# Kernel tuning notes

Hardware: AMD Instinct MI355X
Metric: run time of the kernel (lower is better)

Reference implementation:

```python
import jax, jax.numpy as jnp
import numpy as np

B, D, N = 16, 512, 1024


def setup_inputs() -> dict:
    key = jax.random.key(0)
    k1, k2, k3, k4, k5 = jax.random.split(key, 5)
    return {
        "src_embedding": jax.random.normal(k1, (B, D, N), dtype=jnp.float32),
        "tgt_embedding": jax.random.normal(k2, (B, D, N), dtype=jnp.float32),
        "src": jax.random.normal(k3, (B, 3, N), dtype=jnp.float32),
        "tgt": jax.random.normal(k4, (B, 3, N), dtype=jnp.float32),
        "temperature": jax.random.uniform(k5, (B,), dtype=jnp.float32),
    }


def reference(src_embedding, tgt_embedding, src, tgt, temperature):
    b, d, n = src_embedding.shape
    # scores = softmax(temp * (src_emb^T tgt_emb) / sqrt(d_k), dim=2)
    logits = jnp.einsum("bdn,bdm->bnm", src_embedding, tgt_embedding) / np.sqrt(d).astype(np.float32)
    scores = jax.nn.softmax(temperature.reshape(b, 1, 1) * logits, axis=2)  # [B,N,N]
    # src_corr = tgt @ scores^T  -> soft correspondences [B,3,N]
    src_corr = jnp.einsum("bdm,bnm->bdn", tgt, scores)
    src_mean = src.mean(axis=2, keepdims=True)            # [B,3,1]
    corr_mean = src_corr.mean(axis=2, keepdims=True)      # [B,3,1]
    src_c = src - src_mean
    corr_c = src_corr - corr_mean
    H = jnp.einsum("bin,bjn->bij", src_c, corr_c)         # [B,3,3] covariance
    # Kabsch with reflection fix (batched 3x3 SVD)
    u, s, vh = jnp.linalg.svd(H)
    v = jnp.swapaxes(vh, -1, -2)
    ut = jnp.swapaxes(u, -1, -2)
    det = jax.lax.stop_gradient(jnp.linalg.det(v @ ut))   # +/-1, constant in torch (.item())
    d3 = jnp.stack([jnp.ones_like(det), jnp.ones_like(det), det], axis=-1)  # [B,3]
    R = (v * d3[:, None, :]) @ ut                          # v @ diag(1,1,det) @ u^T
    t = (-R @ src_mean) + corr_mean                        # [B,3,1]
    return R, t.reshape(b, 3)
```

## Files before the change

### kernel.cpp

```cpp
#include <hip/hip_runtime.h>
#include <math.h>

#define BATCH 16
#define DIM 512
#define NPTS 1024

typedef __attribute__((ext_vector_type(8))) short short8;
typedef __attribute__((ext_vector_type(4))) float f32x4;

__device__ __forceinline__ unsigned short f2bf(float x) {
    unsigned u = __float_as_uint(x);
    unsigned r = (u + 0x7FFFu + ((u >> 16) & 1u)) >> 16;
    return (unsigned short)r;
}

__device__ __forceinline__ void load_lds16(const void* g, void* l) {
    __builtin_amdgcn_global_load_lds(
        (const __attribute__((address_space(1))) void*)g,
        (__attribute__((address_space(3))) void*)l, 16, 0, 0);
}

__device__ void kabsch_from_H(double H[3][3], const double sm[3], const double cm[3],
                              float* out, int b) {
    double C[3][3];
    for (int i = 0; i < 3; ++i)
        for (int j = 0; j < 3; ++j) {
            double s = 0;
            for (int k = 0; k < 3; ++k) s += H[k][i] * H[k][j];
            C[i][j] = s;
        }
    double V[3][3] = {{1, 0, 0}, {0, 1, 0}, {0, 0, 1}};
    for (int sweep = 0; sweep < 30; ++sweep) {
        const double offd = fabs(C[0][1]) + fabs(C[0][2]) + fabs(C[1][2]);
        const double diag = fabs(C[0][0]) + fabs(C[1][1]) + fabs(C[2][2]);
        if (offd <= 1e-15 * (diag + 1e-300)) break;
        for (int pq = 0; pq < 3; ++pq) {
            const int p = (pq == 2) ? 1 : 0;
            const int q = (pq == 0) ? 1 : 2;
            const double apq = C[p][q];
            if (fabs(apq) < 1e-300) continue;
            const double theta = (C[q][q] - C[p][p]) / (2.0 * apq);
            const double t_ = copysign(1.0, theta) / (fabs(theta) + sqrt(1.0 + theta * theta));
            const double c_ = 1.0 / sqrt(1.0 + t_ * t_);
            const double s_ = t_ * c_;
            const int r = 3 - p - q;
            const double cpp = C[p][p], cqq = C[q][q];
            C[p][p] = cpp - t_ * apq;
            C[q][q] = cqq + t_ * apq;
            C[p][q] = C[q][p] = 0.0;
            const double crp = C[r][p], crq = C[r][q];
            C[r][p] = C[p][r] = c_ * crp - s_ * crq;
            C[r][q] = C[q][r] = s_ * crp + c_ * crq;
            for (int k = 0; k < 3; ++k) {
                const double vkp = V[k][p], vkq = V[k][q];
                V[k][p] = c_ * vkp - s_ * vkq;
                V[k][q] = s_ * vkp + c_ * vkq;
            }
        }
    }
    double lam[3] = {C[0][0], C[1][1], C[2][2]};
    int i0 = 0, i1 = 1, i2 = 2, tswp;
    if (lam[i0] < lam[i1]) { tswp = i0; i0 = i1; i1 = tswp; }
    if (lam[i0] < lam[i2]) { tswp = i0; i0 = i2; i2 = tswp; }
    if (lam[i1] < lam[i2]) { tswp = i1; i1 = i2; i2 = tswp; }

    const double v0[3] = {V[0][i0], V[1][i0], V[2][i0]};
    const double v1[3] = {V[0][i1], V[1][i1], V[2][i1]};
    const double v2[3] = {V[0][i2], V[1][i2], V[2][i2]};
    const double detV = v0[0] * (v1[1] * v2[2] - v1[2] * v2[1])
                      - v0[1] * (v1[0] * v2[2] - v1[2] * v2[0])
                      + v0[2] * (v1[0] * v2[1] - v1[1] * v2[0]);

    double u0[3], u1[3], u2[3];
    for (int i = 0; i < 3; ++i)
        u0[i] = H[i][0] * v0[0] + H[i][1] * v0[1] + H[i][2] * v0[2];
    double n0 = sqrt(u0[0] * u0[0] + u0[1] * u0[1] + u0[2] * u0[2]);
    n0 = fmax(n0, 1e-300);
    u0[0] /= n0; u0[1] /= n0; u0[2] /= n0;
    for (int i = 0; i < 3; ++i)
        u1[i] = H[i][0] * v1[0] + H[i][1] * v1[1] + H[i][2] * v1[2];
    const double d01 = u0[0] * u1[0] + u0[1] * u1[1] + u0[2] * u1[2];
    u1[0] -= d01 * u0[0]; u1[1] -= d01 * u0[1]; u1[2] -= d01 * u0[2];
    double n1 = sqrt(u1[0] * u1[0] + u1[1] * u1[1] + u1[2] * u1[2]);
    n1 = fmax(n1, 1e-300);
    u1[0] /= n1; u1[1] /= n1; u1[2] /= n1;
    u2[0] = u0[1] * u1[2] - u0[2] * u1[1];
    u2[1] = u0[2] * u1[0] - u0[0] * u1[2];
    u2[2] = u0[0] * u1[1] - u0[1] * u1[0];

    double R[3][3];
    for (int a = 0; a < 3; ++a)
        for (int c = 0; c < 3; ++c)
            R[a][c] = v0[a] * u0[c] + v1[a] * u1[c] + detV * v2[a] * u2[c];

    for (int a = 0; a < 3; ++a) {
        const double tv = cm[a] - (R[a][0] * sm[0] + R[a][1] * sm[1] + R[a][2] * sm[2]);
        out[b * 9 + a * 3 + 0] = (float)R[a][0];
        out[b * 9 + a * 3 + 1] = (float)R[a][1];
        out[b * 9 + a * 3 + 2] = (float)R[a][2];
        out[BATCH * 9 + b * 3 + a] = (float)tv;
    }
}

__global__ __launch_bounds__(256) void transpose_bf16_kernel(
    const float* __restrict__ src_emb, const float* __restrict__ tgt_emb,
    unsigned short* __restrict__ AT, unsigned short* __restrict__ BT)
{
    const int bid = blockIdx.x;
    const int pass = bid & 1;
    const int r2 = bid >> 1;
    const int b  = r2 >> 7;
    const int dt = (r2 >> 4) & 7;
    const int nt = r2 & 15;
    const int tid = threadIdx.x;

    __shared__ float tile[64][65];

    const float* src = pass ? tgt_emb : src_emb;
    unsigned short* dst = pass ? BT : AT;

    const int lr = tid >> 4;
    const int c4 = (tid & 15) * 4;
#pragma unroll
    for (int q = 0; q < 4; ++q) {
        const int dl = lr + q * 16;
        const float4 v = *(const float4*)(src + ((size_t)(b * DIM + dt * 64 + dl)) * NPTS + nt * 64 + c4);
        tile[dl][c4 + 0] = v.x;
        tile[dl][c4 + 1] = v.y;
        tile[dl][c4 + 2] = v.z;
        tile[dl][c4 + 3] = v.w;
    }
    __syncthreads();

#pragma unroll
    for (int s = 0; s < 2; ++s) {
        const int nl = s * 32 + (tid >> 3);
        const int d8 = (tid & 7) * 8;
        union { unsigned short us[8]; uint4 q4; } pk;
#pragma unroll
        for (int k = 0; k < 8; ++k) pk.us[k] = f2bf(tile[d8 + k][nl]);
        *(uint4*)(dst + ((size_t)(b * NPTS + nt * 64 + nl)) * DIM + dt * 64 + d8) = pk.q4;
    }
}

#define AB_BYTES 4096
#define BB_BYTES 16384

__global__ __launch_bounds__(256) void attn_corr_kernel(
    const unsigned short* __restrict__ AT, const unsigned short* __restrict__ BT,
    const float* __restrict__ tgt, const float* __restrict__ temperature,
    float* __restrict__ P)
{
    __shared__ char lds[2 * (AB_BYTES + BB_BYTES)];

    const int bid = blockIdx.x;
    const int slice = bid & 7;
    const int j     = bid >> 3;
    const int pair  = j >> 4;
    const int qt    = j & 15;
    const int pidx  = slice * 8 + pair;
    const int b     = pidx >> 2;
    const int ms    = pidx & 3;

    const int tid = threadIdx.x;
    const int lane = tid & 63;
    const int wv = tid >> 6;

    const unsigned short* Abase = AT + ((size_t)b * NPTS + qt * 64) * DIM;
    const unsigned short* Bbase = BT + ((size_t)b * NPTS + ms * 256) * DIM;

    const int a_r  = wv * 16 + (lane >> 2);
    const int a_cl = (lane & 3) ^ ((a_r >> 1) & 3);
    const size_t a_src_off = (size_t)a_r * DIM + a_cl * 8;

    int b_r[4], b_cl[4];
#pragma unroll
    for (int q = 0; q < 4; ++q) {
        b_r[q]  = q * 64 + wv * 16 + (lane >> 2);
        b_cl[q] = (lane & 3) ^ ((b_r[q] >> 1) & 3);
    }

    const int fp = lane & 15;
    const int fg = lane >> 4;

    const float s2 = temperature[b] * (0.04419417382415922f * 1.4426950408889634f);
    const float* tb = tgt + (size_t)b * 3 * NPTS;
    float tv0[4][4], tv1[4][4], tv2[4][4];
#pragma unroll
    for (int kt = 0; kt < 4; ++kt)
#pragma unroll
        for (int reg = 0; reg < 4; ++reg) {
            const int m = ms * 256 + wv * 64 + kt * 16 + fg * 4 + reg;
            tv0[kt][reg] = tb[m];
            tv1[kt][reg] = tb[NPTS + m];
            tv2[kt][reg] = tb[2 * NPTS + m];
        }
    __builtin_amdgcn_sched_barrier(0);

    f32x4 acc[4][4];
#pragma unroll
    for (int kt = 0; kt < 4; ++kt)
#pragma unroll
        for (int qj = 0; qj < 4; ++qj) acc[kt][qj] = (f32x4){0.f, 0.f, 0.f, 0.f};

    char* AbP[2] = {lds, lds + AB_BYTES};
    char* BbP[2] = {lds + 2 * AB_BYTES, lds + 2 * AB_BYTES + BB_BYTES};

#define STAGE(CH, ABUF, BBUF)                                                        \
    {                                                                                \
        const int d0_ = (CH) * 32;                                                   \
        load_lds16(Abase + a_src_off + d0_, (ABUF) + wv * 1024);                     \
        _Pragma("unroll")                                                            \
        for (int q = 0; q < 4; ++q)                                                  \
            load_lds16(Bbase + (size_t)b_r[q] * DIM + d0_ + b_cl[q] * 8,             \
                       (BBUF) + q * 4096 + wv * 1024);                               \
    }

#define COMPUTE(ABUF, BBUF)                                                          \
    {                                                                                \
        short8 kf[4], qf[4];                                                         \
        _Pragma("unroll")                                                            \
        for (int kt = 0; kt < 4; ++kt) {                                             \
            const int r = wv * 64 + kt * 16 + fp;                                    \
            const int cl = fg ^ ((r >> 1) & 3);                                      \
            kf[kt] = *(const short8*)((BBUF) + r * 64 + cl * 16);                    \
        }                                                                            \
        _Pragma("unroll")                                                            \
        for (int qj = 0; qj < 4; ++qj) {                                             \
            const int r = qj * 16 + fp;                                              \
            const int cl = fg ^ ((r >> 1) & 3);                                      \
            qf[qj] = *(const short8*)((ABUF) + r * 64 + cl * 16);                    \
        }                                                                            \
        __builtin_amdgcn_s_setprio(1);                                               \
        _Pragma("unroll")                                                            \
        for (int kt = 0; kt < 4; ++kt)                                               \
            _Pragma("unroll")                                                        \
            for (int qj = 0; qj < 4; ++qj)                                           \
                acc[kt][qj] = __builtin_amdgcn_mfma_f32_16x16x32_bf16(               \
                    kf[kt], qf[qj], acc[kt][qj], 0, 0, 0);                           \
        __builtin_amdgcn_s_setprio(0);                                               \
    }

    STAGE(0, AbP[0], BbP[0]);
    STAGE(1, AbP[1], BbP[1]);

#pragma unroll
    for (int ch = 0; ch < 16; ++ch) {
        if (ch <= 14) { asm volatile("s_waitcnt vmcnt(5)" ::: "memory"); }
        else          { asm volatile("s_waitcnt vmcnt(0)" ::: "memory"); }
        __builtin_amdgcn_s_barrier();
        __builtin_amdgcn_sched_barrier(0);
        COMPUTE(AbP[ch & 1], BbP[ch & 1]);
        __builtin_amdgcn_sched_barrier(0);
        if (ch < 14) {
            __builtin_amdgcn_s_barrier();
            STAGE(ch + 2, AbP[ch & 1], BbP[ch & 1]);
        }
    }

    float l[4]  = {0.f, 0.f, 0.f, 0.f};
    float a0[4] = {0.f, 0.f, 0.f, 0.f};
    float a1[4] = {0.f, 0.f, 0.f, 0.f};
    float a2[4] = {0.f, 0.f, 0.f, 0.f};

#pragma unroll
    for (int kt = 0; kt < 4; ++kt) {
#pragma unroll
        for (int qj = 0; qj < 4; ++qj) {
#pragma unroll
            for (int reg = 0; reg < 4; ++reg) {
                const float w = exp2f(acc[kt][qj][reg] * s2);
                l[qj]  += w;
                a0[qj] = fmaf(w, tv0[kt][reg], a0[qj]);
                a1[qj] = fmaf(w, tv1[kt][reg], a1[qj]);
                a2[qj] = fmaf(w, tv2[kt][reg], a2[qj]);
            }
        }
    }

    float* Pb = P + ((size_t)b * 16 + (ms * 4 + wv)) * 4 * NPTS;
#pragma unroll
    for (int qj = 0; qj < 4; ++qj) {
        float lv = l[qj], v0 = a0[qj], v1 = a1[qj], v2 = a2[qj];
        lv += __shfl_xor(lv, 16); lv += __shfl_xor(lv, 32);
        v0 += __shfl_xor(v0, 16); v0 += __shfl_xor(v0, 32);
        v1 += __shfl_xor(v1, 16); v1 += __shfl_xor(v1, 32);
        v2 += __shfl_xor(v2, 16); v2 += __shfl_xor(v2, 32);
        if (fg == 0) {
            const int n = qt * 64 + qj * 16 + fp;
            Pb[0 * NPTS + n] = lv;
            Pb[1 * NPTS + n] = v0;
            Pb[2 * NPTS + n] = v1;
            Pb[3 * NPTS + n] = v2;
        }
    }
}

__global__ __launch_bounds__(256) void merge_partial_kernel(
    const float* __restrict__ P, const float* __restrict__ src,
    float* __restrict__ Pacc)
{
    const int bid = blockIdx.x;
    const int b   = bid >> 2;
    const int seg = bid & 3;
    const int tid = threadIdx.x;
    const int n   = seg * 256 + tid;

    const float* Pb = P + (size_t)b * 16 * 4 * NPTS;
    float l = 0, a0 = 0, a1 = 0, a2 = 0;
    for (int pp = 0; pp < 16; ++pp) {
        const float* q = Pb + (size_t)pp * 4 * NPTS;
        l  += q[n];
        a0 += q[NPTS + n];
        a1 += q[2 * NPTS + n];
        a2 += q[3 * NPTS + n];
    }
    const float inv = 1.0f / l;
    const float c0 = a0 * inv, c1 = a1 * inv, c2 = a2 * inv;

    const float* sp = src + (size_t)b * 3 * NPTS;
    const float s0 = sp[n], s1 = sp[NPTS + n], s2 = sp[2 * NPTS + n];

    float v[15] = { s0, s1, s2, c0, c1, c2,
                    s0 * c0, s0 * c1, s0 * c2,
                    s1 * c0, s1 * c1, s1 * c2,
                    s2 * c0, s2 * c1, s2 * c2 };

#pragma unroll
    for (int off = 1; off < 64; off <<= 1)
#pragma unroll
        for (int k = 0; k < 15; ++k) v[k] += __shfl_xor(v[k], off);

    __shared__ float red[4][15];
    const int wv = tid >> 6;
    if ((tid & 63) == 0)
#pragma unroll
        for (int k = 0; k < 15; ++k) red[wv][k] = v[k];
    __syncthreads();
    if (tid < 15)
        Pacc[bid * 15 + tid] = red[0][tid] + red[1][tid] + red[2][tid] + red[3][tid];
}

__global__ __launch_bounds__(64) void svd_final_kernel(
    const float* __restrict__ Pacc, float* __restrict__ out)
{
    const int b = blockIdx.x;
    if (threadIdx.x != 0) return;

    double s[15];
    for (int k = 0; k < 15; ++k) {
        double acc = 0;
        for (int seg = 0; seg < 4; ++seg)
            acc += (double)Pacc[(b * 4 + seg) * 15 + k];
        s[k] = acc;
    }
    const double invN = 1.0 / (double)NPTS;
    const double sm[3] = {s[0] * invN, s[1] * invN, s[2] * invN};
    const double cm[3] = {s[3] * invN, s[4] * invN, s[5] * invN};
    double H[3][3];
    for (int i = 0; i < 3; ++i)
        for (int jj = 0; jj < 3; ++jj)
            H[i][jj] = s[6 + i * 3 + jj] - (double)NPTS * sm[i] * cm[jj];
    kabsch_from_H(H, sm, cm, out, b);
}

__global__ __launch_bounds__(256) void flash_corr_kernel(
    const float* __restrict__ src_emb,
    const float* __restrict__ tgt_emb,
    const float* __restrict__ tgt,
    const float* __restrict__ temperature,
    float* __restrict__ corr)
{
    const int bid = blockIdx.x;
    const int b   = bid & 15;
    const int qt  = bid >> 4;
    const int n0  = qt * 64;
    const int tid = threadIdx.x;
    const int tx  = tid & 15;
    const int ty  = tid >> 4;

    const float scale = temperature[b] * (1.0f / sqrtf((float)DIM));

    __shared__ float As[2][32][64];
    __shared__ float Bs[2][32][64];
    __shared__ float Ts[3][64];

    const float* Abase  = src_emb + (size_t)b * DIM * NPTS + n0;
    const float* Bbatch = tgt_emb + (size_t)b * DIM * NPTS;
    const float* Tbatch = tgt     + (size_t)b * 3 * NPTS;

    const int dr0 = tid >> 4;
    const int dr1 = dr0 + 16;
    const int c4  = (tid & 15) * 4;

    float mrun[4], lpart[4], acc0[4], acc1[4], acc2[4];
#pragma unroll
    for (int r = 0; r < 4; ++r) {
        mrun[r] = -1e30f; lpart[r] = 0.0f;
        acc0[r] = 0.0f; acc1[r] = 0.0f; acc2[r] = 0.0f;
    }

    for (int mt = 0; mt < 16; ++mt) {
        const int m0 = mt * 64;
        const float* Bbase = Bbatch + m0;
        __syncthreads();
        if (tid < 192) {
            const int i = tid >> 6, mc = tid & 63;
            Ts[i][mc] = Tbatch[i * NPTS + m0 + mc];
        }
        {
            float4 a0 = *(const float4*)(Abase + (size_t)dr0 * NPTS + c4);
            float4 a1 = *(const float4*)(Abase + (size_t)dr1 * NPTS + c4);
            float4 b0 = *(const float4*)(Bbase + (size_t)dr0 * NPTS + c4);
            float4 b1 = *(const float4*)(Bbase + (size_t)dr1 * NPTS + c4);
            *(float4*)&As[0][dr0][c4] = a0;
            *(float4*)&As[0][dr1][c4] = a1;
            *(float4*)&Bs[0][dr0][c4] = b0;
            *(float4*)&Bs[0][dr1][c4] = b1;
        }
        __syncthreads();

        float S[4][4];
#pragma unroll
        for (int r = 0; r < 4; ++r)
#pragma unroll
            for (int c = 0; c < 4; ++c) S[r][c] = 0.0f;

        for (int ch = 0; ch < 16; ++ch) {
            const int buf = ch & 1;
            float4 a0n, a1n, b0n, b1n;
            if (ch < 15) {
                const float* Ab = Abase + (size_t)(ch + 1) * 32 * NPTS;
                const float* Bb = Bbase + (size_t)(ch + 1) * 32 * NPTS;
                a0n = *(const float4*)(Ab + (size_t)dr0 * NPTS + c4);
                a1n = *(const float4*)(Ab + (size_t)dr1 * NPTS + c4);
                b0n = *(const float4*)(Bb + (size_t)dr0 * NPTS + c4);
                b1n = *(const float4*)(Bb + (size_t)dr1 * NPTS + c4);
            }
#pragma unroll
            for (int dk = 0; dk < 32; ++dk) {
                const float4 av = *(const float4*)(&As[buf][dk][ty * 4]);
                const float4 bv = *(const float4*)(&Bs[buf][dk][tx * 4]);
                S[0][0] = fmaf(av.x, bv.x, S[0][0]);
                S[0][1] = fmaf(av.x, bv.y, S[0][1]);
                S[0][2] = fmaf(av.x, bv.z, S[0][2]);
                S[0][3] = fmaf(av.x, bv.w, S[0][3]);
                S[1][0] = fmaf(av.y, bv.x, S[1][0]);
                S[1][1] = fmaf(av.y, bv.y, S[1][1]);
                S[1][2] = fmaf(av.y, bv.z, S[1][2]);
                S[1][3] = fmaf(av.y, bv.w, S[1][3]);
                S[2][0] = fmaf(av.z, bv.x, S[2][0]);
                S[2][1] = fmaf(av.z, bv.y, S[2][1]);
                S[2][2] = fmaf(av.z, bv.z, S[2][2]);
                S[2][3] = fmaf(av.z, bv.w, S[2][3]);
                S[3][0] = fmaf(av.w, bv.x, S[3][0]);
                S[3][1] = fmaf(av.w, bv.y, S[3][1]);
                S[3][2] = fmaf(av.w, bv.z, S[3][2]);
                S[3][3] = fmaf(av.w, bv.w, S[3][3]);
            }
            __syncthreads();
            if (ch < 15) {
                *(float4*)&As[buf ^ 1][dr0][c4] = a0n;
                *(float4*)&As[buf ^ 1][dr1][c4] = a1n;
                *(float4*)&Bs[buf ^ 1][dr0][c4] = b0n;
                *(float4*)&Bs[buf ^ 1][dr1][c4] = b1n;
                __syncthreads();
            }
        }

#pragma unroll
        for (int r = 0; r < 4; ++r) {
            float z0 = S[r][0] * scale, z1 = S[r][1] * scale;
            float z2 = S[r][2] * scale, z3 = S[r][3] * scale;
            float mt_ = fmaxf(fmaxf(z0, z1), fmaxf(z2, z3));
#pragma unroll
            for (int off = 1; off < 16; off <<= 1)
                mt_ = fmaxf(mt_, __shfl_xor(mt_, off));
            const float mnew = fmaxf(mrun[r], mt_);
            const float f = expf(mrun[r] - mnew);
            lpart[r] *= f; acc0[r] *= f; acc1[r] *= f; acc2[r] *= f;
            const float w0 = expf(z0 - mnew);
            const float w1 = expf(z1 - mnew);
            const float w2 = expf(z2 - mnew);
            const float w3 = expf(z3 - mnew);
            lpart[r] += w0 + w1 + w2 + w3;
            const int mc = tx * 4;
            acc0[r] += w0 * Ts[0][mc] + w1 * Ts[0][mc+1] + w2 * Ts[0][mc+2] + w3 * Ts[0][mc+3];
            acc1[r] += w0 * Ts[1][mc] + w1 * Ts[1][mc+1] + w2 * Ts[1][mc+2] + w3 * Ts[1][mc+3];
            acc2[r] += w0 * Ts[2][mc] + w1 * Ts[2][mc+1] + w2 * Ts[2][mc+2] + w3 * Ts[2][mc+3];
            mrun[r] = mnew;
        }
    }

#pragma unroll
    for (int r = 0; r < 4; ++r) {
        float l = lpart[r], a0 = acc0[r], a1 = acc1[r], a2 = acc2[r];
#pragma unroll
        for (int off = 1; off < 16; off <<= 1) {
            l  += __shfl_xor(l,  off);
            a0 += __shfl_xor(a0, off);
            a1 += __shfl_xor(a1, off);
            a2 += __shfl_xor(a2, off);
        }
        if (tx == 0) {
            const int n = n0 + ty * 4 + r;
            const float inv = 1.0f / l;
            corr[((size_t)b * 3 + 0) * NPTS + n] = a0 * inv;
            corr[((size_t)b * 3 + 1) * NPTS + n] = a1 * inv;
            corr[((size_t)b * 3 + 2) * NPTS + n] = a2 * inv;
        }
    }
}

__global__ __launch_bounds__(256) void reduce_svd_kernel(
    const float* __restrict__ src,
    const float* __restrict__ corr,
    float* __restrict__ out)
{
    const int b = blockIdx.x;
    const int tid = threadIdx.x;

    __shared__ float wred[4][9];
    __shared__ float meansh[6];

    const float* sp = src  + (size_t)b * 3 * NPTS;
    const float* cp = corr + (size_t)b * 3 * NPTS;

    float ss0 = 0, ss1 = 0, ss2 = 0, cs0 = 0, cs1 = 0, cs2 = 0;
    for (int n = tid; n < NPTS; n += 256) {
        ss0 += sp[n]; ss1 += sp[NPTS + n]; ss2 += sp[2 * NPTS + n];
        cs0 += cp[n]; cs1 += cp[NPTS + n]; cs2 += cp[2 * NPTS + n];
    }
#pragma unroll
    for (int off = 1; off < 64; off <<= 1) {
        ss0 += __shfl_xor(ss0, off); ss1 += __shfl_xor(ss1, off); ss2 += __shfl_xor(ss2, off);
        cs0 += __shfl_xor(cs0, off); cs1 += __shfl_xor(cs1, off); cs2 += __shfl_xor(cs2, off);
    }
    const int wave = tid >> 6;
    if ((tid & 63) == 0) {
        wred[wave][0] = ss0; wred[wave][1] = ss1; wred[wave][2] = ss2;
        wred[wave][3] = cs0; wred[wave][4] = cs1; wred[wave][5] = cs2;
    }
    __syncthreads();
    if (tid < 6)
        meansh[tid] = (wred[0][tid] + wred[1][tid] + wred[2][tid] + wred[3][tid]) * (1.0f / NPTS);
    __syncthreads();
    const float sm0 = meansh[0], sm1 = meansh[1], sm2 = meansh[2];
    const float cm0 = meansh[3], cm1 = meansh[4], cm2 = meansh[5];

    float h[9] = {0, 0, 0, 0, 0, 0, 0, 0, 0};
    for (int n = tid; n < NPTS; n += 256) {
        const float a0 = sp[n] - sm0, a1 = sp[NPTS + n] - sm1, a2 = sp[2 * NPTS + n] - sm2;
        const float b0 = cp[n] - cm0, b1 = cp[NPTS + n] - cm1, b2 = cp[2 * NPTS + n] - cm2;
        h[0] += a0 * b0; h[1] += a0 * b1; h[2] += a0 * b2;
        h[3] += a1 * b0; h[4] += a1 * b1; h[5] += a1 * b2;
        h[6] += a2 * b0; h[7] += a2 * b1; h[8] += a2 * b2;
    }
#pragma unroll
    for (int off = 1; off < 64; off <<= 1) {
#pragma unroll
        for (int j = 0; j < 9; ++j) h[j] += __shfl_xor(h[j], off);
    }
    __syncthreads();
    if ((tid & 63) == 0) {
#pragma unroll
        for (int j = 0; j < 9; ++j) wred[wave][j] = h[j];
    }
    __syncthreads();

    if (tid == 0) {
        double H[3][3];
        for (int i = 0; i < 3; ++i)
            for (int j = 0; j < 3; ++j)
                H[i][j] = (double)wred[0][i * 3 + j] + wred[1][i * 3 + j]
                        + wred[2][i * 3 + j] + wred[3][i * 3 + j];
        const double sm[3] = {sm0, sm1, sm2};
        const double cm[3] = {cm0, cm1, cm2};
        kabsch_from_H(H, sm, cm, out, b);
    }
}

extern "C" void kernel_launch(void* const* d_in, const int* in_sizes, int n_in,
                              void* d_out, int out_size, void* d_ws, size_t ws_size,
                              hipStream_t stream) {
    const float* src_emb = (const float*)d_in[0];
    const float* tgt_emb = (const float*)d_in[1];
    const float* src     = (const float*)d_in[2];
    const float* tgt     = (const float*)d_in[3];
    const float* temp    = (const float*)d_in[4];
    float* out = (float*)d_out;

    const size_t AT_BYTES   = (size_t)BATCH * NPTS * DIM * 2;
    const size_t P_BYTES    = (size_t)BATCH * 16 * 4 * NPTS * 4;
    const size_t PACC_BYTES = 64 * 15 * sizeof(float);

    if (ws_size >= 2 * AT_BYTES + P_BYTES + PACC_BYTES) {
        unsigned short* AT = (unsigned short*)d_ws;
        unsigned short* BT = (unsigned short*)((char*)d_ws + AT_BYTES);
        float* P    = (float*)((char*)d_ws + 2 * AT_BYTES);
        float* Pacc = (float*)((char*)d_ws + 2 * AT_BYTES + P_BYTES);

        transpose_bf16_kernel<<<dim3(2 * BATCH * 8 * 16), dim3(256), 0, stream>>>(
            src_emb, tgt_emb, AT, BT);
        attn_corr_kernel<<<dim3(BATCH * 16 * 4), dim3(256), 0, stream>>>(
            AT, BT, tgt, temp, P);
        merge_partial_kernel<<<dim3(64), dim3(256), 0, stream>>>(P, src, Pacc);
        svd_final_kernel<<<dim3(BATCH), dim3(64), 0, stream>>>(Pacc, out);
    } else {
        float* corr = (float*)d_ws;
        flash_corr_kernel<<<dim3(BATCH * (NPTS / 64)), dim3(256), 0, stream>>>(
            src_emb, tgt_emb, tgt, temp, corr);
        reduce_svd_kernel<<<dim3(BATCH), dim3(256), 0, stream>>>(src, corr, out);
    }
}
```

Measured before the change: 59.75 us.

## Double query tile to 128 rows and use triple-buffered LDS pipeline

Each attention block now handles 128 query rows instead of 64, so every B-tile load from LDS feeds twice as many MFMAs, and the grid shrinks from 1024 to 512 blocks. The LDS ring goes from two to three stages, which lets the next stage be issued before compute and drops one barrier per iteration. The tgt coordinate loads move after the main loop as float4 loads. The cost is a doubled accumulator register footprint and fewer blocks, which may reduce occupancy and leave CUs underfilled on a 256-CU part.

```diff
diff --git a/kernel.cpp b/kernel.cpp
--- a/kernel.cpp
+++ b/kernel.cpp
@@ -143,7 +143,7 @@
     }
 }
 
-#define AB_BYTES 4096
+#define AB_BYTES 8192
 #define BB_BYTES 16384
 
 __global__ __launch_bounds__(256) void attn_corr_kernel(
@@ -151,13 +151,13 @@
     const float* __restrict__ tgt, const float* __restrict__ temperature,
     float* __restrict__ P)
 {
-    __shared__ char lds[2 * (AB_BYTES + BB_BYTES)];
+    __shared__ char lds[3 * (AB_BYTES + BB_BYTES)];
 
     const int bid = blockIdx.x;
     const int slice = bid & 7;
     const int j     = bid >> 3;
-    const int pair  = j >> 4;
-    const int qt    = j & 15;
+    const int pair  = j >> 3;
+    const int qt    = j & 7;
     const int pidx  = slice * 8 + pair;
     const int b     = pidx >> 2;
     const int ms    = pidx & 3;
@@ -166,13 +166,15 @@
     const int lane = tid & 63;
     const int wv = tid >> 6;
 
-    const unsigned short* Abase = AT + ((size_t)b * NPTS + qt * 64) * DIM;
+    const unsigned short* Abase = AT + ((size_t)b * NPTS + qt * 128) * DIM;
     const unsigned short* Bbase = BT + ((size_t)b * NPTS + ms * 256) * DIM;
 
-    const int a_r  = wv * 16 + (lane >> 2);
-    const int a_cl = (lane & 3) ^ ((a_r >> 1) & 3);
-    const size_t a_src_off = (size_t)a_r * DIM + a_cl * 8;
-
+    int a_r[2], a_cl[2];
+#pragma unroll
+    for (int q = 0; q < 2; ++q) {
+        a_r[q]  = q * 64 + wv * 16 + (lane >> 2);
+        a_cl[q] = (lane & 3) ^ ((a_r[q] >> 1) & 3);
+    }
     int b_r[4], b_cl[4];
 #pragma unroll
     for (int q = 0; q < 4; ++q) {
@@ -183,33 +185,24 @@
     const int fp = lane & 15;
     const int fg = lane >> 4;
 
-    const float s2 = temperature[b] * (0.04419417382415922f * 1.4426950408889634f);
-    const float* tb = tgt + (size_t)b * 3 * NPTS;
-    float tv0[4][4], tv1[4][4], tv2[4][4];
+    f32x4 acc[4][8];
 #pragma unroll
     for (int kt = 0; kt < 4; ++kt)
 #pragma unroll
-        for (int reg = 0; reg < 4; ++reg) {
-            const int m = ms * 256 + wv * 64 + kt * 16 + fg * 4 + reg;
-            tv0[kt][reg] = tb[m];
-            tv1[kt][reg] = tb[NPTS + m];
-            tv2[kt][reg] = tb[2 * NPTS + m];
-        }
-    __builtin_amdgcn_sched_barrier(0);
-
-    f32x4 acc[4][4];
-#pragma unroll
-    for (int kt = 0; kt < 4; ++kt)
-#pragma unroll
-        for (int qj = 0; qj < 4; ++qj) acc[kt][qj] = (f32x4){0.f, 0.f, 0.f, 0.f};
-
-    char* AbP[2] = {lds, lds + AB_BYTES};
-    char* BbP[2] = {lds + 2 * AB_BYTES, lds + 2 * AB_BYTES + BB_BYTES};
+        for (int qj = 0; qj < 8; ++qj) acc[kt][qj] = (f32x4){0.f, 0.f, 0.f, 0.f};
+
+    char* AbP[3] = {lds, lds + AB_BYTES, lds + 2 * AB_BYTES};
+    char* BbP[3] = {lds + 3 * AB_BYTES,
+                    lds + 3 * AB_BYTES + BB_BYTES,
+                    lds + 3 * AB_BYTES + 2 * BB_BYTES};
 
 #define STAGE(CH, ABUF, BBUF)                                                        \
     {                                                                                \
         const int d0_ = (CH) * 32;                                                   \
-        load_lds16(Abase + a_src_off + d0_, (ABUF) + wv * 1024);                     \
+        _Pragma("unroll")                                                            \
+        for (int q = 0; q < 2; ++q)                                                  \
+            load_lds16(Abase + (size_t)a_r[q] * DIM + d0_ + a_cl[q] * 8,             \
+                       (ABUF) + q * 4096 + wv * 1024);                               \
         _Pragma("unroll")                                                            \
         for (int q = 0; q < 4; ++q)                                                  \
             load_lds16(Bbase + (size_t)b_r[q] * DIM + d0_ + b_cl[q] * 8,             \
@@ -218,7 +211,7 @@
 
 #define COMPUTE(ABUF, BBUF)                                                          \
     {                                                                                \
-        short8 kf[4], qf[4];                                                         \
+        short8 kf[4], qf[8];                                                         \
         _Pragma("unroll")                                                            \
         for (int kt = 0; kt < 4; ++kt) {                                             \
             const int r = wv * 64 + kt * 16 + fp;                                    \
@@ -226,7 +219,7 @@
             kf[kt] = *(const short8*)((BBUF) + r * 64 + cl * 16);                    \
         }                                                                            \
         _Pragma("unroll")                                                            \
-        for (int qj = 0; qj < 4; ++qj) {                                             \
+        for (int qj = 0; qj < 8; ++qj) {                                             \
             const int r = qj * 16 + fp;                                              \
             const int cl = fg ^ ((r >> 1) & 3);                                      \
             qf[qj] = *(const short8*)((ABUF) + r * 64 + cl * 16);                    \
@@ -235,7 +228,7 @@
         _Pragma("unroll")                                                            \
         for (int kt = 0; kt < 4; ++kt)                                               \
             _Pragma("unroll")                                                        \
-            for (int qj = 0; qj < 4; ++qj)                                           \
+            for (int qj = 0; qj < 8; ++qj)                                           \
                 acc[kt][qj] = __builtin_amdgcn_mfma_f32_16x16x32_bf16(               \
                     kf[kt], qf[qj], acc[kt][qj], 0, 0, 0);                           \
         __builtin_amdgcn_s_setprio(0);                                               \
@@ -246,27 +239,34 @@
 
 #pragma unroll
     for (int ch = 0; ch < 16; ++ch) {
-        if (ch <= 14) { asm volatile("s_waitcnt vmcnt(5)" ::: "memory"); }
+        if (ch <= 14) { asm volatile("s_waitcnt vmcnt(6)" ::: "memory"); }
         else          { asm volatile("s_waitcnt vmcnt(0)" ::: "memory"); }
         __builtin_amdgcn_s_barrier();
         __builtin_amdgcn_sched_barrier(0);
-        COMPUTE(AbP[ch & 1], BbP[ch & 1]);
+        if (ch + 2 < 16) STAGE(ch + 2, AbP[(ch + 2) % 3], BbP[(ch + 2) % 3]);
+        COMPUTE(AbP[ch % 3], BbP[ch % 3]);
         __builtin_amdgcn_sched_barrier(0);
-        if (ch < 14) {
-            __builtin_amdgcn_s_barrier();
-            STAGE(ch + 2, AbP[ch & 1], BbP[ch & 1]);
-        }
-    }
-
-    float l[4]  = {0.f, 0.f, 0.f, 0.f};
-    float a0[4] = {0.f, 0.f, 0.f, 0.f};
-    float a1[4] = {0.f, 0.f, 0.f, 0.f};
-    float a2[4] = {0.f, 0.f, 0.f, 0.f};
-
+    }
+
+    const float s2 = temperature[b] * (0.04419417382415922f * 1.4426950408889634f);
+    const float* tb = tgt + (size_t)b * 3 * NPTS;
+    float tv0[4][4], tv1[4][4], tv2[4][4];
 #pragma unroll
     for (int kt = 0; kt < 4; ++kt) {
-#pragma unroll
-        for (int qj = 0; qj < 4; ++qj) {
+        const int m0 = ms * 256 + wv * 64 + kt * 16 + fg * 4;
+        *(float4*)tv0[kt] = *(const float4*)(tb + m0);
+        *(float4*)tv1[kt] = *(const float4*)(tb + NPTS + m0);
+        *(float4*)tv2[kt] = *(const float4*)(tb + 2 * NPTS + m0);
+    }
+
+    float l[8], a0[8], a1[8], a2[8];
+#pragma unroll
+    for (int qj = 0; qj < 8; ++qj) { l[qj] = 0.f; a0[qj] = 0.f; a1[qj] = 0.f; a2[qj] = 0.f; }
+
+#pragma unroll
+    for (int kt = 0; kt < 4; ++kt) {
+#pragma unroll
+        for (int qj = 0; qj < 8; ++qj) {
 #pragma unroll
             for (int reg = 0; reg < 4; ++reg) {
                 const float w = exp2f(acc[kt][qj][reg] * s2);
@@ -280,14 +280,14 @@
 
     float* Pb = P + ((size_t)b * 16 + (ms * 4 + wv)) * 4 * NPTS;
 #pragma unroll
-    for (int qj = 0; qj < 4; ++qj) {
+    for (int qj = 0; qj < 8; ++qj) {
         float lv = l[qj], v0 = a0[qj], v1 = a1[qj], v2 = a2[qj];
         lv += __shfl_xor(lv, 16); lv += __shfl_xor(lv, 32);
         v0 += __shfl_xor(v0, 16); v0 += __shfl_xor(v0, 32);
         v1 += __shfl_xor(v1, 16); v1 += __shfl_xor(v1, 32);
         v2 += __shfl_xor(v2, 16); v2 += __shfl_xor(v2, 32);
         if (fg == 0) {
-            const int n = qt * 64 + qj * 16 + fp;
+            const int n = qt * 128 + qj * 16 + fp;
             Pb[0 * NPTS + n] = lv;
             Pb[1 * NPTS + n] = v0;
             Pb[2 * NPTS + n] = v1;
@@ -602,7 +602,7 @@
 
         transpose_bf16_kernel<<<dim3(2 * BATCH * 8 * 16), dim3(256), 0, stream>>>(
             src_emb, tgt_emb, AT, BT);
-        attn_corr_kernel<<<dim3(BATCH * 16 * 4), dim3(256), 0, stream>>>(
+        attn_corr_kernel<<<dim3(BATCH * 8 * 4), dim3(256), 0, stream>>>(
             AT, BT, tgt, temp, P);
         merge_partial_kernel<<<dim3(64), dim3(256), 0, stream>>>(P, src, Pacc);
         svd_final_kernel<<<dim3(BATCH), dim3(64), 0, stream>>>(Pacc, out);
```

Result: faster. 58.11 us (median of 2 runs) (-2.8%).
